# Optimization experiments

Measured on AMD Instinct MI355X. Metric: run time of the kernel, lower is better.

## Reference

```python
import jax, jax.numpy as jnp
import numpy as np

B, R, D, P = 32, 512, 256, 5532  # images, rois/image, feat dim, num_pids
NEG_INF = -1e30

def setup_inputs() -> dict:
    key = jax.random.key(0)
    k1, k2, k3 = jax.random.split(key, 3)
    inputs = jax.random.normal(k1, (B * R, D), dtype=jnp.float32)
    cls_scores = jax.random.uniform(k2, (B * R, 1), dtype=jnp.float32)
    roi_label = jax.random.randint(k3, (B, R), 0, P + 1)  # 0 = background -> label -1
    return {"inputs": inputs, "cls_scores": cls_scores, "roi_label": roi_label}

def reference(inputs, cls_scores, roi_label):
    x = (inputs * cls_scores).reshape(B, R, D)          # scale features by cls score
    label = roi_label - 1                               # [B,R], -1 = background
    valid = label >= 0                                  # keep labeled ROIs only
    lbl = jnp.where(valid, label, 0)

    # per-image per-pid mean prototypes via one segmented reduction
    seg = (jnp.arange(B)[:, None] * P + lbl).reshape(-1)             # [B*R]
    w = valid.reshape(-1).astype(x.dtype)
    sums = jax.ops.segment_sum(x.reshape(-1, D) * w[:, None], seg, num_segments=B * P)
    counts = jax.ops.segment_sum(w, seg, num_segments=B * P)          # [B*P]
    proto = sums / jnp.maximum(counts, 1.0)[:, None]
    proto = proto / jnp.maximum(jnp.linalg.norm(proto, axis=-1, keepdims=True), 1e-12)
    proto = jax.lax.stop_gradient(proto).reshape(B, P, D)            # .detach() in torch
    present = (counts > 0).reshape(B, P)                              # unique labels per image

    # project each ROI feature onto its image's prototypes
    logits = jnp.einsum('brd,bpd->brp', x, proto)                     # [B,R,P]
    logits = jnp.where(present[:, None, :], logits, NEG_INF)          # softmax over unique labels only
    logp = jax.nn.log_softmax(logits, axis=-1)
    nll = -jnp.take_along_axis(logp, lbl[..., None], axis=-1)[..., 0] # [B,R]
    nll = jnp.where(valid, nll, 0.0)
    n_valid = jnp.maximum(jnp.sum(valid).astype(x.dtype), 1.0)
    return jnp.sum(nll) / n_valid
```

## Files before the change

### kernel.cpp

```cpp
#include <hip/hip_runtime.h>
#include <math.h>

#define Bn 32
#define Rn 512
#define Dn 256
#define Pn 5532
#define MAXU 512
#define NEGBIG -3.0e38f

typedef short short8 __attribute__((ext_vector_type(8)));
typedef short short4v __attribute__((ext_vector_type(4)));
typedef float floatx4 __attribute__((ext_vector_type(4)));

#define COUNTS_OFF   0
#define NLL_OFF      (Bn*Pn)
#define ZERO_WORDS   (NLL_OFF + 4)
#define XBF_OFF      ZERO_WORDS
#define XBF_WORDS    (Bn*Rn*Dn/2)
#define PBF_OFF      (XBF_OFF + XBF_WORDS)
#define PBF_WORDS    (Bn*MAXU*Dn/2)
#define CMAP_OFF     (PBF_OFF + PBF_WORDS)
#define CCNT_OFF     (CMAP_OFF + Bn*Pn)
#define CURS_OFF     (CCNT_OFF + Bn*MAXU)
#define RLIST_OFF    (CURS_OFF + Bn*MAXU)
#define NUNIQ_OFF    (RLIST_OFF + Bn*Rn)
#define NVALID_OFF   (NUNIQ_OFF + 32)
#define MPART_OFF    (NVALID_OFF + 32)
#define SPART_OFF    (MPART_OFF + Bn*Rn*4)
#define DLBL_OFF     (SPART_OFF + Bn*Rn*4)

__device__ __forceinline__ unsigned short bf16r(float f) {
    union { float f; unsigned int u; } c; c.f = f;
    return (unsigned short)((c.u + 0x7FFFu + ((c.u >> 16) & 1u)) >> 16);
}

__device__ __forceinline__ void async16(void* lds, const void* g) {
    auto* l3 = reinterpret_cast<__attribute__((address_space(3))) unsigned int*>(
                   reinterpret_cast<size_t>(lds));
    auto* g1 = reinterpret_cast<const __attribute__((address_space(1))) unsigned int*>(
                   reinterpret_cast<size_t>(g));
    __builtin_amdgcn_global_load_lds(g1, l3, 16, 0, 0);
}

__global__ __launch_bounds__(256) void k_prep(const float* __restrict__ inputs,
                                              const float* __restrict__ cls,
                                              unsigned short* __restrict__ xbf) {
    int i8 = blockIdx.x * 256 + threadIdx.x;
    int e = i8 * 8;
    int row = e >> 8;
    float cw = cls[row];
    float4 v0 = *(const float4*)&inputs[e];
    float4 v1 = *(const float4*)&inputs[e + 4];
    short8 o;
    o[0] = (short)bf16r(v0.x * cw); o[1] = (short)bf16r(v0.y * cw);
    o[2] = (short)bf16r(v0.z * cw); o[3] = (short)bf16r(v0.w * cw);
    o[4] = (short)bf16r(v1.x * cw); o[5] = (short)bf16r(v1.y * cw);
    o[6] = (short)bf16r(v1.z * cw); o[7] = (short)bf16r(v1.w * cw);
    *(short8*)&xbf[e] = o;
}

__global__ void k_count(const int* __restrict__ roi_label,
                        int* __restrict__ counts) {
    int i = blockIdx.x * blockDim.x + threadIdx.x;
    if (i >= Bn * Rn) return;
    int b = i >> 9;
    int lbl = roi_label[i] - 1;
    if (lbl >= 0) atomicAdd(&counts[b * Pn + lbl], 1);
}

__global__ __launch_bounds__(1024) void k_compact(
    const int* __restrict__ counts, int* __restrict__ nuniq,
    int* __restrict__ cmap, int* __restrict__ ccnt,
    int* __restrict__ cursor, int* __restrict__ nvalid_arr) {
    const int b = blockIdx.x;
    const int t = threadIdx.x;
    const int lane = t & 63, wid = t >> 6;
    __shared__ int wpres[16], wcnt[16];
    int basePres = 0, baseCnt = 0;
    for (int i0 = 0; i0 < Pn; i0 += 1024) {
        int i = i0 + t;
        int cnt = (i < Pn) ? counts[b * Pn + i] : 0;
        bool pres = cnt > 0;
        unsigned long long mask = __ballot(pres);
        int pfx_pres = __popcll(mask & ((1ULL << lane) - 1ULL));
        int v = cnt;
        #pragma unroll
        for (int off = 1; off < 64; off <<= 1) {
            int u = __shfl_up(v, off);
            if (lane >= off) v += u;
        }
        int pfx_cnt = v - cnt;
        if (lane == 63) { wpres[wid] = __popcll(mask); wcnt[wid] = v; }
        __syncthreads();
        int woffP = 0, totP = 0, woffC = 0, totC = 0;
        #pragma unroll
        for (int w = 0; w < 16; ++w) {
            int p = wpres[w], c = wcnt[w];
            if (w < wid) { woffP += p; woffC += c; }
            totP += p; totC += c;
        }
        if (pres) {
            int c = basePres + woffP + pfx_pres;
            cmap[b * Pn + i] = c;
            ccnt[b * MAXU + c] = cnt;
            cursor[b * MAXU + c] = baseCnt + woffC + pfx_cnt;
        }
        basePres += totP; baseCnt += totC;
        __syncthreads();
    }
    if (t == 0) { nuniq[b] = basePres; nvalid_arr[b] = baseCnt; }
}

__global__ void k_fill(const int* __restrict__ roi_label, const int* __restrict__ cmap,
                       int* __restrict__ cursor, int* __restrict__ rlist) {
    int i = blockIdx.x * blockDim.x + threadIdx.x;
    int b = i >> 9;
    int lbl = roi_label[i] - 1;
    if (lbl < 0) return;
    int c = cmap[b * Pn + lbl];
    int pos = atomicAdd(&cursor[b * MAXU + c], 1);
    rlist[b * Rn + pos] = i & 511;
}

__global__ __launch_bounds__(64) void k_proto(
    const float* __restrict__ inputs, const float* __restrict__ cls,
    const int* __restrict__ nuniq, const int* __restrict__ ccnt,
    const int* __restrict__ cursor, const int* __restrict__ rlist,
    unsigned short* __restrict__ pbf) {
    int slot = blockIdx.x;
    int b = slot >> 9;
    int c = slot & (MAXU - 1);
    if (c >= nuniq[b]) return;
    int cnt = ccnt[slot];
    int start = cursor[slot] - cnt;
    int t = threadIdx.x;
    float4 acc = make_float4(0.f, 0.f, 0.f, 0.f);
    for (int k = 0; k < cnt; ++k) {
        int r = rlist[b * Rn + start + k];
        float cw = cls[b * Rn + r];
        float4 v = *(const float4*)&inputs[(size_t)(b * Rn + r) * Dn + t * 4];
        acc.x += v.x * cw; acc.y += v.y * cw; acc.z += v.z * cw; acc.w += v.w * cw;
    }
    float inv = 1.0f / (float)cnt;
    acc.x *= inv; acc.y *= inv; acc.z *= inv; acc.w *= inv;
    float ss = acc.x*acc.x + acc.y*acc.y + acc.z*acc.z + acc.w*acc.w;
    #pragma unroll
    for (int off = 32; off > 0; off >>= 1) ss += __shfl_xor(ss, off);
    float scale = 1.0f / fmaxf(sqrtf(ss), 1e-12f);
    short4v o;
    o[0] = (short)bf16r(acc.x * scale); o[1] = (short)bf16r(acc.y * scale);
    o[2] = (short)bf16r(acc.z * scale); o[3] = (short)bf16r(acc.w * scale);
    *(short4v*)&pbf[(size_t)slot * Dn + t * 4] = o;
}

#define TRr 64
#define TCc 128
#define KCk 32

__global__ __launch_bounds__(256, 4) void k_loss(
    const unsigned short* __restrict__ xbf, const unsigned short* __restrict__ pbf,
    const int* __restrict__ roi_label, const int* __restrict__ cmap,
    const int* __restrict__ nuniq,
    float* __restrict__ mpart, float* __restrict__ spart,
    float* __restrict__ dlbl_arr)
{
    __shared__ __align__(16) unsigned short xs[2][TRr * KCk];
    __shared__ __align__(16) unsigned short ps[2][TCc * KCk];
    __shared__ int lblc[TRr];
    __shared__ float mw[4][TRr], sw[4][TRr];

    const int t = threadIdx.x;
    const int lane = t & 63, w = t >> 6;
    const int q = lane >> 4, r15 = lane & 15;
    const int b = blockIdx.z;
    const int pc = blockIdx.y;
    const int roiBase = blockIdx.x * TRr;
    const int U = nuniq[b];
    if (pc * TCc >= U) return;

    if (t < TRr) {
        int lbl = roi_label[b * Rn + roiBase + t] - 1;
        lblc[t] = (lbl >= 0) ? cmap[b * Pn + lbl] : -1;
    }

    const int s0 = w * 64 + lane;
    const int xrow = s0 >> 2;
    const int xg = (s0 & 3) ^ ((xrow >> 1) & 3);
    const size_t xgbase = (size_t)(b * Rn + roiBase + xrow) * Dn + xg * 8;
    int prow[2], pg[2];
    #pragma unroll
    for (int cc = 0; cc < 2; ++cc) {
        int s = (w + cc * 4) * 64 + lane;
        prow[cc] = s >> 2;
        pg[cc] = (s & 3) ^ ((prow[cc] >> 1) & 3);
    }

    #define ISSUE(kc, buf)                                                        \
        do {                                                                      \
            async16(&xs[buf][w * 512], xbf + xgbase + (kc) * KCk);                \
            async16(&ps[buf][w * 512],                                            \
                    pbf + (size_t)(b * MAXU + pc * TCc + prow[0]) * Dn            \
                        + (kc) * KCk + pg[0] * 8);                                \
            async16(&ps[buf][(w + 4) * 512],                                      \
                    pbf + (size_t)(b * MAXU + pc * TCc + prow[1]) * Dn            \
                        + (kc) * KCk + pg[1] * 8);                                \
        } while (0)

    ISSUE(0, 0);

    floatx4 acc[4][2];
    #pragma unroll
    for (int mt = 0; mt < 4; ++mt)
        #pragma unroll
        for (int nt = 0; nt < 2; ++nt) acc[mt][nt] = (floatx4)0.f;

    for (int kc = 0; kc < Dn / KCk; ++kc) {
        const int cur = kc & 1;
        __syncthreads();
        if (kc < Dn / KCk - 1) ISSUE(kc + 1, cur ^ 1);

        short8 a[4], bb[2];
        #pragma unroll
        for (int mt = 0; mt < 4; ++mt) {
            int row = mt * 16 + r15;
            int off = row * KCk + ((q ^ ((row >> 1) & 3)) * 8);
            a[mt] = *(const short8*)&xs[cur][off];
        }
        #pragma unroll
        for (int nt = 0; nt < 2; ++nt) {
            int row = w * 32 + nt * 16 + r15;
            int off = row * KCk + ((q ^ ((row >> 1) & 3)) * 8);
            bb[nt] = *(const short8*)&ps[cur][off];
        }
        #pragma unroll
        for (int mt = 0; mt < 4; ++mt)
            #pragma unroll
            for (int nt = 0; nt < 2; ++nt)
                acc[mt][nt] = __builtin_amdgcn_mfma_f32_16x16x32_bf16(a[mt], bb[nt], acc[mt][nt], 0, 0, 0);
    }

    const int c0 = pc * TCc + w * 32 + r15;
    const int c1 = c0 + 16;
    const bool v0 = c0 < U, v1 = c1 < U;
    #pragma unroll
    for (int mt = 0; mt < 4; ++mt)
        #pragma unroll
        for (int reg = 0; reg < 4; ++reg) {
            int mloc = mt * 16 + q * 4 + reg;
            float d0 = acc[mt][0][reg], d1 = acc[mt][1][reg];
            int lc = lblc[mloc];
            if (v0 && c0 == lc) dlbl_arr[b * Rn + roiBase + mloc] = d0;
            if (v1 && c1 == lc) dlbl_arr[b * Rn + roiBase + mloc] = d1;
            float M = fmaxf(v0 ? d0 : NEGBIG, v1 ? d1 : NEGBIG);
            #pragma unroll
            for (int off = 1; off < 16; off <<= 1) M = fmaxf(M, __shfl_xor(M, off));
            float s = (v0 ? __expf(d0 - M) : 0.f) + (v1 ? __expf(d1 - M) : 0.f);
            #pragma unroll
            for (int off = 1; off < 16; off <<= 1) s += __shfl_xor(s, off);
            if (r15 == 0) { mw[w][mloc] = M; sw[w][mloc] = s; }
        }
    __syncthreads();

    if (t < TRr) {
        float M = fmaxf(fmaxf(mw[0][t], mw[1][t]), fmaxf(mw[2][t], mw[3][t]));
        float s = 0.f;
        #pragma unroll
        for (int wv = 0; wv < 4; ++wv) s += sw[wv][t] * __expf(mw[wv][t] - M);
        int roi = b * Rn + roiBase + t;
        mpart[roi * 4 + pc] = M;
        spart[roi * 4 + pc] = s;
    }
    #undef ISSUE
}

__global__ __launch_bounds__(256) void k_merge(
    const int* __restrict__ roi_label, const int* __restrict__ nuniq,
    const float* __restrict__ mpart, const float* __restrict__ spart,
    const float* __restrict__ dlbl_arr, float* __restrict__ nll_sum)
{
    __shared__ float wsum[4];
    int roi = blockIdx.x * 256 + threadIdx.x;
    int b = roi >> 9;
    int lbl = roi_label[roi] - 1;
    float v = 0.f;
    if (lbl >= 0) {
        int U = nuniq[b];
        int nch = (U + TCc - 1) / TCc;
        float m = NEGBIG, s = 0.f;
        for (int pc = 0; pc < nch; ++pc) {
            float om = mpart[roi * 4 + pc], os = spart[roi * 4 + pc];
            float M = fmaxf(m, om);
            s = s * __expf(m - M) + os * __expf(om - M);
            m = M;
        }
        v = m + __logf(s) - dlbl_arr[roi];
    }
    #pragma unroll
    for (int off = 1; off < 64; off <<= 1) v += __shfl_xor(v, off);
    int lane = threadIdx.x & 63, wid = threadIdx.x >> 6;
    if (lane == 0) wsum[wid] = v;
    __syncthreads();
    if (threadIdx.x == 0)
        atomicAdd(nll_sum, wsum[0] + wsum[1] + wsum[2] + wsum[3]);
}

__global__ void k_final(const float* __restrict__ nll_sum,
                        const int* __restrict__ nvalid_arr, float* __restrict__ out) {
    int s = 0;
    #pragma unroll
    for (int b = 0; b < Bn; ++b) s += nvalid_arr[b];
    out[0] = nll_sum[0] / fmaxf((float)s, 1.0f);
}

extern "C" void kernel_launch(void* const* d_in, const int* in_sizes, int n_in,
                              void* d_out, int out_size, void* d_ws, size_t ws_size,
                              hipStream_t stream) {
    const float* inputs = (const float*)d_in[0];
    const float* cls    = (const float*)d_in[1];
    const int*   roi    = (const int*)d_in[2];
    float* out = (float*)d_out;

    float* wsf = (float*)d_ws;
    int*   wsi = (int*)d_ws;
    int*   counts = wsi + COUNTS_OFF;
    float* nll    = wsf + NLL_OFF;
    unsigned short* xbf = (unsigned short*)(wsi + XBF_OFF);
    unsigned short* pbf = (unsigned short*)(wsi + PBF_OFF);
    int*   cmap   = wsi + CMAP_OFF;
    int*   ccnt   = wsi + CCNT_OFF;
    int*   cursor = wsi + CURS_OFF;
    int*   rlist  = wsi + RLIST_OFF;
    int*   nuniq  = wsi + NUNIQ_OFF;
    int*   nvalid = wsi + NVALID_OFF;
    float* mpart  = wsf + MPART_OFF;
    float* spart  = wsf + SPART_OFF;
    float* dlbl   = wsf + DLBL_OFF;

    hipMemsetAsync(d_ws, 0, (size_t)ZERO_WORDS * 4, stream);
    k_count  <<<(Bn*Rn)/256, 256, 0, stream>>>(roi, counts);
    k_prep   <<<(Bn*Rn*Dn)/(256*8), 256, 0, stream>>>(inputs, cls, xbf);
    k_compact<<<Bn, 1024, 0, stream>>>(counts, nuniq, cmap, ccnt, cursor, nvalid);
    k_fill   <<<(Bn*Rn)/256, 256, 0, stream>>>(roi, cmap, cursor, rlist);
    k_proto  <<<Bn*MAXU, 64, 0, stream>>>(inputs, cls, nuniq, ccnt, cursor, rlist, pbf);
    dim3 g(Rn / TRr, 4, Bn);
    k_loss   <<<g, 256, 0, stream>>>(xbf, pbf, roi, cmap, nuniq, mpart, spart, dlbl);
    k_merge  <<<(Bn*Rn)/256, 256, 0, stream>>>(roi, nuniq, mpart, spart, dlbl, nll);
    k_final  <<<1, 1, 0, stream>>>(nll, nvalid, out);
}
```

Measured before the change: 120.0 us.

## Fuse count, fill and final kernels, and enlarge the loss ROI tile to 128

Label counting moves into k_prep. The ROI-list fill moves into k_compact, which now keeps cmap and the cursors in LDS and uses LDS atomics. The final division moves into k_merge behind a last-block ticket. Together this removes three kernel launches and some global atomic traffic. k_loss now processes 128 ROIs per block with twice the accumulators and occupancy hint 3, so each prototype tile loaded into LDS is reused across more rows. The cost is higher register pressure and half as many loss blocks.

New measurement: 115.6 us. 1.04x faster.

```diff
diff --git a/kernel.cpp b/kernel.cpp
--- a/kernel.cpp
+++ b/kernel.cpp
@@ -14,7 +14,8 @@
 
 #define COUNTS_OFF   0
 #define NLL_OFF      (Bn*Pn)
-#define ZERO_WORDS   (NLL_OFF + 4)
+#define TICKET_OFF   (NLL_OFF + 1)
+#define ZERO_WORDS   (TICKET_OFF + 3)
 #define XBF_OFF      ZERO_WORDS
 #define XBF_WORDS    (Bn*Rn*Dn/2)
 #define PBF_OFF      (XBF_OFF + XBF_WORDS)
@@ -44,8 +45,15 @@
 
 __global__ __launch_bounds__(256) void k_prep(const float* __restrict__ inputs,
                                               const float* __restrict__ cls,
-                                              unsigned short* __restrict__ xbf) {
+                                              const int* __restrict__ roi_label,
+                                              unsigned short* __restrict__ xbf,
+                                              int* __restrict__ counts) {
     int i8 = blockIdx.x * 256 + threadIdx.x;
+    if (i8 < Bn * Rn) {
+        int b = i8 >> 9;
+        int lbl = roi_label[i8] - 1;
+        if (lbl >= 0) atomicAdd(&counts[b * Pn + lbl], 1);
+    }
     int e = i8 * 8;
     int row = e >> 8;
     float cw = cls[row];
@@ -59,23 +67,16 @@
     *(short8*)&xbf[e] = o;
 }
 
-__global__ void k_count(const int* __restrict__ roi_label,
-                        int* __restrict__ counts) {
-    int i = blockIdx.x * blockDim.x + threadIdx.x;
-    if (i >= Bn * Rn) return;
-    int b = i >> 9;
-    int lbl = roi_label[i] - 1;
-    if (lbl >= 0) atomicAdd(&counts[b * Pn + lbl], 1);
-}
-
 __global__ __launch_bounds__(1024) void k_compact(
-    const int* __restrict__ counts, int* __restrict__ nuniq,
-    int* __restrict__ cmap, int* __restrict__ ccnt,
-    int* __restrict__ cursor, int* __restrict__ nvalid_arr) {
+    const int* __restrict__ roi_label, const int* __restrict__ counts,
+    int* __restrict__ nuniq, int* __restrict__ cmap, int* __restrict__ ccnt,
+    int* __restrict__ cursor, int* __restrict__ rlist, int* __restrict__ nvalid_arr) {
     const int b = blockIdx.x;
     const int t = threadIdx.x;
     const int lane = t & 63, wid = t >> 6;
     __shared__ int wpres[16], wcnt[16];
+    __shared__ int cmap_lds[Pn];
+    __shared__ int curs_lds[MAXU];
     int basePres = 0, baseCnt = 0;
     for (int i0 = 0; i0 < Pn; i0 += 1024) {
         int i = i0 + t;
@@ -101,25 +102,26 @@
         }
         if (pres) {
             int c = basePres + woffP + pfx_pres;
+            cmap_lds[i] = c;
             cmap[b * Pn + i] = c;
             ccnt[b * MAXU + c] = cnt;
-            cursor[b * MAXU + c] = baseCnt + woffC + pfx_cnt;
+            curs_lds[c] = baseCnt + woffC + pfx_cnt;
         }
         basePres += totP; baseCnt += totC;
         __syncthreads();
     }
+    if (t < Rn) {
+        int lbl = roi_label[b * Rn + t] - 1;
+        if (lbl >= 0) {
+            int c = cmap_lds[lbl];
+            int pos = atomicAdd(&curs_lds[c], 1);
+            rlist[b * Rn + pos] = t;
+        }
+    }
+    __syncthreads();
+    if (t < MAXU && t < basePres)
+        cursor[b * MAXU + t] = curs_lds[t];
     if (t == 0) { nuniq[b] = basePres; nvalid_arr[b] = baseCnt; }
-}
-
-__global__ void k_fill(const int* __restrict__ roi_label, const int* __restrict__ cmap,
-                       int* __restrict__ cursor, int* __restrict__ rlist) {
-    int i = blockIdx.x * blockDim.x + threadIdx.x;
-    int b = i >> 9;
-    int lbl = roi_label[i] - 1;
-    if (lbl < 0) return;
-    int c = cmap[b * Pn + lbl];
-    int pos = atomicAdd(&cursor[b * MAXU + c], 1);
-    rlist[b * Rn + pos] = i & 511;
 }
 
 __global__ __launch_bounds__(64) void k_proto(
@@ -153,11 +155,11 @@
     *(short4v*)&pbf[(size_t)slot * Dn + t * 4] = o;
 }
 
-#define TRr 64
+#define TRr 128
 #define TCc 128
 #define KCk 32
 
-__global__ __launch_bounds__(256, 4) void k_loss(
+__global__ __launch_bounds__(256, 3) void k_loss(
     const unsigned short* __restrict__ xbf, const unsigned short* __restrict__ pbf,
     const int* __restrict__ roi_label, const int* __restrict__ cmap,
     const int* __restrict__ nuniq,
@@ -183,34 +185,35 @@
         lblc[t] = (lbl >= 0) ? cmap[b * Pn + lbl] : -1;
     }
 
-    const int s0 = w * 64 + lane;
-    const int xrow = s0 >> 2;
-    const int xg = (s0 & 3) ^ ((xrow >> 1) & 3);
-    const size_t xgbase = (size_t)(b * Rn + roiBase + xrow) * Dn + xg * 8;
-    int prow[2], pg[2];
+    int xrow[2], xg[2], prow[2], pg[2];
     #pragma unroll
     for (int cc = 0; cc < 2; ++cc) {
         int s = (w + cc * 4) * 64 + lane;
-        prow[cc] = s >> 2;
-        pg[cc] = (s & 3) ^ ((prow[cc] >> 1) & 3);
-    }
-
-    #define ISSUE(kc, buf)                                                        \
-        do {                                                                      \
-            async16(&xs[buf][w * 512], xbf + xgbase + (kc) * KCk);                \
-            async16(&ps[buf][w * 512],                                            \
-                    pbf + (size_t)(b * MAXU + pc * TCc + prow[0]) * Dn            \
-                        + (kc) * KCk + pg[0] * 8);                                \
-            async16(&ps[buf][(w + 4) * 512],                                      \
-                    pbf + (size_t)(b * MAXU + pc * TCc + prow[1]) * Dn            \
-                        + (kc) * KCk + pg[1] * 8);                                \
+        xrow[cc] = s >> 2; xg[cc] = (s & 3) ^ ((xrow[cc] >> 1) & 3);
+        prow[cc] = s >> 2; pg[cc] = xg[cc];
+    }
+
+    #define ISSUE(kc, buf)                                                         \
+        do {                                                                       \
+            async16(&xs[buf][w * 512],                                             \
+                    xbf + (size_t)(b * Rn + roiBase + xrow[0]) * Dn                \
+                        + (kc) * KCk + xg[0] * 8);                                 \
+            async16(&xs[buf][(w + 4) * 512],                                       \
+                    xbf + (size_t)(b * Rn + roiBase + xrow[1]) * Dn                \
+                        + (kc) * KCk + xg[1] * 8);                                 \
+            async16(&ps[buf][w * 512],                                             \
+                    pbf + (size_t)(b * MAXU + pc * TCc + prow[0]) * Dn             \
+                        + (kc) * KCk + pg[0] * 8);                                 \
+            async16(&ps[buf][(w + 4) * 512],                                       \
+                    pbf + (size_t)(b * MAXU + pc * TCc + prow[1]) * Dn             \
+                        + (kc) * KCk + pg[1] * 8);                                 \
         } while (0)
 
     ISSUE(0, 0);
 
-    floatx4 acc[4][2];
-    #pragma unroll
-    for (int mt = 0; mt < 4; ++mt)
+    floatx4 acc[8][2];
+    #pragma unroll
+    for (int mt = 0; mt < 8; ++mt)
         #pragma unroll
         for (int nt = 0; nt < 2; ++nt) acc[mt][nt] = (floatx4)0.f;
 
@@ -219,13 +222,7 @@
         __syncthreads();
         if (kc < Dn / KCk - 1) ISSUE(kc + 1, cur ^ 1);
 
-        short8 a[4], bb[2];
-        #pragma unroll
-        for (int mt = 0; mt < 4; ++mt) {
-            int row = mt * 16 + r15;
-            int off = row * KCk + ((q ^ ((row >> 1) & 3)) * 8);
-            a[mt] = *(const short8*)&xs[cur][off];
-        }
+        short8 bb[2];
         #pragma unroll
         for (int nt = 0; nt < 2; ++nt) {
             int row = w * 32 + nt * 16 + r15;
@@ -233,17 +230,20 @@
             bb[nt] = *(const short8*)&ps[cur][off];
         }
         #pragma unroll
-        for (int mt = 0; mt < 4; ++mt)
-            #pragma unroll
-            for (int nt = 0; nt < 2; ++nt)
-                acc[mt][nt] = __builtin_amdgcn_mfma_f32_16x16x32_bf16(a[mt], bb[nt], acc[mt][nt], 0, 0, 0);
+        for (int mt = 0; mt < 8; ++mt) {
+            int row = mt * 16 + r15;
+            int off = row * KCk + ((q ^ ((row >> 1) & 3)) * 8);
+            short8 a = *(const short8*)&xs[cur][off];
+            acc[mt][0] = __builtin_amdgcn_mfma_f32_16x16x32_bf16(a, bb[0], acc[mt][0], 0, 0, 0);
+            acc[mt][1] = __builtin_amdgcn_mfma_f32_16x16x32_bf16(a, bb[1], acc[mt][1], 0, 0, 0);
+        }
     }
 
     const int c0 = pc * TCc + w * 32 + r15;
     const int c1 = c0 + 16;
     const bool v0 = c0 < U, v1 = c1 < U;
     #pragma unroll
-    for (int mt = 0; mt < 4; ++mt)
+    for (int mt = 0; mt < 8; ++mt)
         #pragma unroll
         for (int reg = 0; reg < 4; ++reg) {
             int mloc = mt * 16 + q * 4 + reg;
@@ -276,7 +276,9 @@
 __global__ __launch_bounds__(256) void k_merge(
     const int* __restrict__ roi_label, const int* __restrict__ nuniq,
     const float* __restrict__ mpart, const float* __restrict__ spart,
-    const float* __restrict__ dlbl_arr, float* __restrict__ nll_sum)
+    const float* __restrict__ dlbl_arr, float* __restrict__ nll_sum,
+    int* __restrict__ ticket, const int* __restrict__ nvalid_arr,
+    float* __restrict__ out)
 {
     __shared__ float wsum[4];
     int roi = blockIdx.x * 256 + threadIdx.x;
@@ -300,16 +302,18 @@
     int lane = threadIdx.x & 63, wid = threadIdx.x >> 6;
     if (lane == 0) wsum[wid] = v;
     __syncthreads();
-    if (threadIdx.x == 0)
+    if (threadIdx.x == 0) {
         atomicAdd(nll_sum, wsum[0] + wsum[1] + wsum[2] + wsum[3]);
-}
-
-__global__ void k_final(const float* __restrict__ nll_sum,
-                        const int* __restrict__ nvalid_arr, float* __restrict__ out) {
-    int s = 0;
-    #pragma unroll
-    for (int b = 0; b < Bn; ++b) s += nvalid_arr[b];
-    out[0] = nll_sum[0] / fmaxf((float)s, 1.0f);
+        __threadfence();
+        int tk = atomicAdd(ticket, 1);
+        if (tk == gridDim.x - 1) {
+            __threadfence();
+            int s = 0;
+            #pragma unroll
+            for (int bb = 0; bb < Bn; ++bb) s += nvalid_arr[bb];
+            out[0] = nll_sum[0] / fmaxf((float)s, 1.0f);
+        }
+    }
 }
 
 extern "C" void kernel_launch(void* const* d_in, const int* in_sizes, int n_in,
@@ -324,6 +328,7 @@
     int*   wsi = (int*)d_ws;
     int*   counts = wsi + COUNTS_OFF;
     float* nll    = wsf + NLL_OFF;
+    int*   ticket = wsi + TICKET_OFF;
     unsigned short* xbf = (unsigned short*)(wsi + XBF_OFF);
     unsigned short* pbf = (unsigned short*)(wsi + PBF_OFF);
     int*   cmap   = wsi + CMAP_OFF;
@@ -337,13 +342,11 @@
     float* dlbl   = wsf + DLBL_OFF;
 
     hipMemsetAsync(d_ws, 0, (size_t)ZERO_WORDS * 4, stream);
-    k_count  <<<(Bn*Rn)/256, 256, 0, stream>>>(roi, counts);
-    k_prep   <<<(Bn*Rn*Dn)/(256*8), 256, 0, stream>>>(inputs, cls, xbf);
-    k_compact<<<Bn, 1024, 0, stream>>>(counts, nuniq, cmap, ccnt, cursor, nvalid);
-    k_fill   <<<(Bn*Rn)/256, 256, 0, stream>>>(roi, cmap, cursor, rlist);
+    k_prep   <<<(Bn*Rn*Dn)/(256*8), 256, 0, stream>>>(inputs, cls, roi, xbf, counts);
+    k_compact<<<Bn, 1024, 0, stream>>>(roi, counts, nuniq, cmap, ccnt, cursor, rlist, nvalid);
     k_proto  <<<Bn*MAXU, 64, 0, stream>>>(inputs, cls, nuniq, ccnt, cursor, rlist, pbf);
     dim3 g(Rn / TRr, 4, Bn);
     k_loss   <<<g, 256, 0, stream>>>(xbf, pbf, roi, cmap, nuniq, mpart, spart, dlbl);
-    k_merge  <<<(Bn*Rn)/256, 256, 0, stream>>>(roi, nuniq, mpart, spart, dlbl, nll);
-    k_final  <<<1, 1, 0, stream>>>(nll, nvalid, out);
-}
+    k_merge  <<<(Bn*Rn)/256, 256, 0, stream>>>(roi, nuniq, mpart, spart, dlbl, nll,
+                                               ticket, nvalid, out);
+}
```
